# Kernel tuning notes

Hardware: AMD Instinct MI355X
Metric: run time of the kernel (lower is better)

Reference implementation:

```python
import jax, jax.numpy as jnp
import numpy as np

N = 2048
H = 128
W = 128
NEAR = 0.1


def _quat_to_rotmat(q):
    # q: [N,4] (w,x,y,z), normalized -> [N,3,3]
    q = q / jnp.clip(jnp.linalg.norm(q, axis=1, keepdims=True), 1e-8)
    w, x, y, z = q[:, 0], q[:, 1], q[:, 2], q[:, 3]
    xx, yy, zz = x * x, y * y, z * z
    xy, xz, yz = x * y, x * z, y * z
    wx, wy, wz = w * x, w * y, w * z
    r0 = jnp.stack([1 - 2 * (yy + zz), 2 * (xy - wz), 2 * (xz + wy)], axis=1)
    r1 = jnp.stack([2 * (xy + wz), 1 - 2 * (xx + zz), 2 * (yz - wx)], axis=1)
    r2 = jnp.stack([2 * (xz - wy), 2 * (yz + wx), 1 - 2 * (xx + yy)], axis=1)
    return jnp.stack([r0, r1, r2], axis=1)


def _covariance_matrices(log_scales, rotations):
    # R diag(s^2) R^T + 1e-6 I, per Gaussian
    s2 = jnp.exp(2.0 * log_scales)  # scales**2
    R = _quat_to_rotmat(rotations)  # [N,3,3]
    cov = jnp.einsum('nij,nj,nkj->nik', R, s2, R)
    return cov + 1e-6 * jnp.eye(3, dtype=cov.dtype)


def _render(means, cov3d, colors, opacities, intrinsics, camera_to_world, height, width):
    dt = means.dtype
    Rcw = camera_to_world[:3, :3]
    tcw = camera_to_world[:3, 3]
    Rwc = Rcw.T
    twc = -Rwc @ tcw
    p = means @ Rwc.T + twc  # [N,3] camera-space
    x, y, z = p[:, 0], p[:, 1], p[:, 2]
    valid = (z > NEAR).astype(dt)
    zc = jnp.maximum(z, NEAR)
    fx, fy = intrinsics[0, 0], intrinsics[1, 1]
    cx, cy = intrinsics[0, 2], intrinsics[1, 2]
    u = fx * x / zc + cx
    v = fy * y / zc + cy
    # EWA projection Jacobian [N,2,3]
    zeros = jnp.zeros_like(zc)
    J0 = jnp.stack([fx / zc, zeros, -fx * x / (zc * zc)], axis=1)
    J1 = jnp.stack([zeros, fy / zc, -fy * y / (zc * zc)], axis=1)
    J = jnp.stack([J0, J1], axis=1)
    cov_cam = jnp.einsum('ij,njk,lk->nil', Rwc, cov3d, Rwc)  # [N,3,3]
    cov2d = jnp.einsum('nij,njk,nlk->nil', J, cov_cam, J) + 0.3 * jnp.eye(2, dtype=dt)
    a, b, c = cov2d[:, 0, 0], cov2d[:, 0, 1], cov2d[:, 1, 1]
    det = jnp.maximum(a * c - b * b, 1e-12)
    cA, cB, cC = c / det, -b / det, a / det  # conic (inverse 2D covariance)
    # front-to-back depth order; invalid Gaussians pushed to the back
    order = jnp.argsort(jnp.where(valid > 0, zc, jnp.inf))
    u, v = u[order], v[order]
    cA, cB, cC = cA[order], cB[order], cC[order]
    op = (opacities * valid)[order]
    cols = colors[order]
    xs = jnp.arange(width, dtype=dt)
    ys = jnp.arange(height, dtype=dt)
    dx = xs[None, None, :] - u[:, None, None]  # [N,1,W] -> broadcasts
    dy = ys[None, :, None] - v[:, None, None]  # [N,H,1]
    power = (-0.5 * (cA[:, None, None] * dx * dx + cC[:, None, None] * dy * dy)
             - cB[:, None, None] * dx * dy)  # [N,H,W]
    power = jnp.minimum(power, 0.0)
    alpha = jnp.clip(op[:, None, None] * jnp.exp(power), 0.0, 0.99)
    Tcum = jnp.cumprod(1.0 - alpha, axis=0)
    Texcl = jnp.concatenate([jnp.ones_like(Tcum[:1]), Tcum[:-1]], axis=0)
    weight = alpha * Texcl  # [N,H,W]
    img = jnp.einsum('nhw,nc->hwc', weight, cols)  # [H,W,3]
    return img


def setup_inputs():
    key = jax.random.key(0)
    k = jax.random.split(key, 6)
    xy = jax.random.uniform(k[0], (N, 2), minval=-2.0, maxval=2.0)
    z = jax.random.uniform(k[1], (N, 1), minval=3.0, maxval=9.0)
    means = jnp.concatenate([xy, z], axis=1)
    log_scales = jnp.log(jax.random.uniform(k[2], (N, 3), minval=0.02, maxval=0.2))
    rotations = jax.random.normal(k[3], (N, 4))
    colors = jax.random.uniform(k[4], (N, 3))
    opacities = jax.random.normal(k[5], (N,))
    intrinsics = jnp.array([[150.0, 0.0, W / 2], [0.0, 150.0, H / 2], [0.0, 0.0, 1.0]], dtype=jnp.float32)
    camera_to_world = jnp.eye(4, dtype=jnp.float32)
    return {"means": means, "log_scales": log_scales, "rotations": rotations,
            "colors": colors, "opacities": opacities, "intrinsics": intrinsics,
            "camera_to_world": camera_to_world, "height": H, "width": W}


def reference(means, log_scales, rotations, colors, opacities, intrinsics, camera_to_world, height, width):
    cov3d = _covariance_matrices(log_scales, rotations)
    return _render(means, cov3d, jnp.clip(colors, 0.0, 1.0), jax.nn.sigmoid(opacities),
                   intrinsics, camera_to_world, height, width)
```

## Files before the change

### kernel.cpp

```cpp
#include <hip/hip_runtime.h>
#include <hip/hip_bf16.h>

#define NMAX 2048
#define HH 128
#define WW 128
#define NSEG 16
#define SEG 128
#define NEARP 0.1f
#define CULL_LOG_EPS -18.0f

static __device__ __forceinline__ float ldin(const void* p, int i, bool is32) {
    return is32 ? ((const float*)p)[i]
                : __bfloat162float(((const __hip_bfloat16*)p)[i]);
}
static __device__ __forceinline__ bool detect32(const void* intr) {
    return ((const float*)intr)[0] > 1.0f;
}
static __device__ __forceinline__ void stout(void* out, int i, float v, bool is32) {
    if (is32) ((float*)out)[i] = v;
    else      ((__hip_bfloat16*)out)[i] = __float2bfloat16(v);
}


__global__ __launch_bounds__(256) void gs_preprocess(
    const void* __restrict__ means,
    const void* __restrict__ log_scales,
    const void* __restrict__ rots,
    const void* __restrict__ colors,
    const void* __restrict__ opac,
    const void* __restrict__ intr,
    const void* __restrict__ c2w,
    int n,
    unsigned long long* __restrict__ keys,
    float* __restrict__ params)
{
    int i = blockIdx.x * blockDim.x + threadIdx.x;
    if (i >= NMAX) return;
    bool is32 = detect32(intr);
    if (i >= n) {
        keys[i] = (((unsigned long long)0x7f800000u) << 32) | (unsigned int)i;
        return;
    }

    float Rwc[3][3], twc[3];
    {
        float Rcw[3][3], tcw[3];
        for (int r = 0; r < 3; ++r) {
            for (int c = 0; c < 3; ++c) Rcw[r][c] = ldin(c2w, r * 4 + c, is32);
            tcw[r] = ldin(c2w, r * 4 + 3, is32);
        }
        for (int r = 0; r < 3; ++r)
            for (int c = 0; c < 3; ++c) Rwc[r][c] = Rcw[c][r];
        for (int r = 0; r < 3; ++r)
            twc[r] = -(Rwc[r][0] * tcw[0] + Rwc[r][1] * tcw[1] + Rwc[r][2] * tcw[2]);
    }
    float fx = ldin(intr, 0, is32), fy = ldin(intr, 4, is32);
    float cx = ldin(intr, 2, is32), cy = ldin(intr, 5, is32);

    float mx = ldin(means, 3 * i, is32), my = ldin(means, 3 * i + 1, is32),
          mz = ldin(means, 3 * i + 2, is32);
    float px = Rwc[0][0] * mx + Rwc[0][1] * my + Rwc[0][2] * mz + twc[0];
    float py = Rwc[1][0] * mx + Rwc[1][1] * my + Rwc[1][2] * mz + twc[1];
    float pz = Rwc[2][0] * mx + Rwc[2][1] * my + Rwc[2][2] * mz + twc[2];
    bool valid = pz > NEARP;
    float zc = fmaxf(pz, NEARP);
    float izc = 1.0f / zc;
    float u = fx * px * izc + cx;
    float v = fy * py * izc + cy;

    float qw = ldin(rots, 4 * i, is32), qx = ldin(rots, 4 * i + 1, is32),
          qy = ldin(rots, 4 * i + 2, is32), qz = ldin(rots, 4 * i + 3, is32);
    float nrm = sqrtf(qw * qw + qx * qx + qy * qy + qz * qz);
    float inv = 1.0f / fmaxf(nrm, 1e-8f);
    qw *= inv; qx *= inv; qy *= inv; qz *= inv;
    float xx = qx * qx, yy = qy * qy, zz = qz * qz;
    float xy = qx * qy, xz = qx * qz, yz = qy * qz;
    float wx = qw * qx, wy = qw * qy, wz = qw * qz;
    float R[3][3] = {
        {1.f - 2.f * (yy + zz), 2.f * (xy - wz),       2.f * (xz + wy)},
        {2.f * (xy + wz),       1.f - 2.f * (xx + zz), 2.f * (yz - wx)},
        {2.f * (xz - wy),       2.f * (yz + wx),       1.f - 2.f * (xx + yy)}
    };
    float s2[3];
    for (int k = 0; k < 3; ++k) s2[k] = __expf(2.0f * ldin(log_scales, 3 * i + k, is32));

    float M[3][3];
    for (int r = 0; r < 3; ++r)
        for (int c = 0; c < 3; ++c)
            M[r][c] = R[r][0] * s2[0] * R[c][0] + R[r][1] * s2[1] * R[c][1]
                    + R[r][2] * s2[2] * R[c][2];
    M[0][0] += 1e-6f; M[1][1] += 1e-6f; M[2][2] += 1e-6f;

    float TM[3][3];
    for (int r = 0; r < 3; ++r)
        for (int c = 0; c < 3; ++c)
            TM[r][c] = Rwc[r][0] * M[0][c] + Rwc[r][1] * M[1][c] + Rwc[r][2] * M[2][c];
    float CC[3][3];
    for (int r = 0; r < 3; ++r)
        for (int c = 0; c < 3; ++c)
            CC[r][c] = TM[r][0] * Rwc[c][0] + TM[r][1] * Rwc[c][1] + TM[r][2] * Rwc[c][2];

    float J0[3] = {fx * izc, 0.0f, -fx * px * izc * izc};
    float J1[3] = {0.0f, fy * izc, -fy * py * izc * izc};
    float t0[3], t1[3];
    for (int c = 0; c < 3; ++c) {
        t0[c] = J0[0] * CC[0][c] + J0[1] * CC[1][c] + J0[2] * CC[2][c];
        t1[c] = J1[0] * CC[0][c] + J1[1] * CC[1][c] + J1[2] * CC[2][c];
    }
    float a  = t0[0] * J0[0] + t0[1] * J0[1] + t0[2] * J0[2] + 0.3f;
    float bq = t0[0] * J1[0] + t0[1] * J1[1] + t0[2] * J1[2];
    float cq = t1[0] * J1[0] + t1[1] * J1[1] + t1[2] * J1[2] + 0.3f;
    float det = fmaxf(a * cq - bq * bq, 1e-12f);
    float idet = 1.0f / det;
    float cA = cq * idet, cB = -bq * idet, cCc = a * idet;

    float o  = ldin(opac, i, is32);
    float op = valid ? (1.0f / (1.0f + __expf(-o))) : 0.0f;
    float cr = fminf(fmaxf(ldin(colors, 3 * i, is32), 0.f), 1.f);
    float cg = fminf(fmaxf(ldin(colors, 3 * i + 1, is32), 0.f), 1.f);
    float cb = fminf(fmaxf(ldin(colors, 3 * i + 2, is32), 0.f), 1.f);

    float zkey = valid ? zc : __builtin_inff();
    keys[i] = (((unsigned long long)__float_as_uint(zkey)) << 32) | (unsigned int)i;

    float na  = -0.5f * cA;
    float nb  = -cB;
    float ncc = -0.5f * cCc;
    float qyb = ncc - nb * nb / (4.0f * na);
    float qxb = na  - nb * nb / (4.0f * ncc);
    float lnop = __logf(op);

    float* p = params + i * 12;
    p[0] = u;  p[1] = v;
    p[2] = na;  p[3] = nb;  p[4] = ncc;
    p[5] = op;
    p[6] = cr; p[7] = cg; p[8] = cb;
    p[9] = qyb; p[10] = lnop; p[11] = qxb;
}

__global__ __launch_bounds__(256) void gs_rank_scatter(
    const unsigned long long* __restrict__ keys_in,
    const float* __restrict__ params_in,
    float* __restrict__ params_sorted,
    int n)
{
    __shared__ unsigned long long sk[NMAX];
    __shared__ int pr[32][9];
    __shared__ int rk[32];
    int t = threadIdx.x;
    #pragma unroll
    for (int e = 0; e < 8; ++e) sk[t + e * 256] = keys_in[t + e * 256];
    __syncthreads();

    int g0 = blockIdx.x * 32;
    int gi = t >> 3;
    int c  = t & 7;
    unsigned long long mykey = sk[g0 + gi];
    int cnt = 0;
    #pragma unroll 8
    for (int j = c; j < NMAX; j += 8)
        cnt += (sk[j] < mykey) ? 1 : 0;
    pr[gi][c] = cnt;
    __syncthreads();

    if (t < 32) {
        int r = 0;
        #pragma unroll
        for (int k = 0; k < 8; ++k) r += pr[t][k];
        rk[t] = r;
    }
    __syncthreads();

    if (t < 96) {
        int g = t / 3, q = t % 3;
        int src = g0 + g;
        float4 val;
        if (src < n) val = ((const float4*)params_in)[src * 3 + q];
        else         val = make_float4(0.f, 0.f, 0.f, 0.f);
        ((float4*)params_sorted)[rk[g] * 3 + q] = val;
    }
}

__global__ __launch_bounds__(256) void gs_render(
    const float* __restrict__ params_sorted,
    float4* __restrict__ segbuf)
{
    __shared__ float sp[SEG * 12];
    __shared__ int swcnt[2];
    int seg = blockIdx.y;
    int t = threadIdx.x;
    int x0 = (blockIdx.x & 3) * 32;
    int y0 = (blockIdx.x >> 2) * 16;

    float4 a4, b4, c4;
    bool keep = false;
    if (t < SEG) {
        const float4* src = (const float4*)(params_sorted + (seg * SEG + t) * 12);
        a4 = src[0];
        b4 = src[1];
        c4 = src[2];
        float dxm = fmaxf(fmaxf((float)x0 - a4.x, a4.x - (float)(x0 + 31)), 0.0f);
        float dym = fmaxf(fmaxf((float)y0 - a4.y, a4.y - (float)(y0 + 15)), 0.0f);
        float bound = fminf(c4.y * dym * dym, c4.w * dxm * dxm) + c4.z;
        keep = (bound > CULL_LOG_EPS) && (b4.y > 0.0f);
    }
    unsigned long long ball = __ballot(keep);
    int lane = t & 63, wid = t >> 6;
    if (lane == 0 && wid < 2) swcnt[wid] = (int)__popcll(ball);
    __syncthreads();
    int M = swcnt[0] + swcnt[1];
    if (keep) {
        int rank = (wid ? swcnt[0] : 0)
                 + (int)__popcll(ball & ((1ull << lane) - 1ull));
        float4* d = (float4*)(sp + rank * 12);
        d[0] = a4; d[1] = b4; d[2] = c4;
    }
    __syncthreads();

    int col = x0 + ((t & 15) << 1);
    int row = y0 + (t >> 4);
    float px0 = (float)col;
    float px1 = px0 + 1.0f;
    float py  = (float)row;
    int pid0 = row * WW + col;

    float T0 = 1.f, r0 = 0.f, g0 = 0.f, b0 = 0.f;
    float T1 = 1.f, r1 = 0.f, g1 = 0.f, b1 = 0.f;
    #pragma unroll 2
    for (int i = 0; i < M; ++i) {
        const float* gp = sp + i * 12;
        float4 A = *(const float4*)(gp);
        float4 B = *(const float4*)(gp + 4);
        float4 C = *(const float4*)(gp + 8);
        float dy    = py - A.y;
        float nbdy  = A.w * dy;
        float ncdy2 = (B.x * dy) * dy;

        float dx0 = px0 - A.x;
        float p0 = fmaf(fmaf(A.z, dx0, nbdy), dx0, ncdy2);
        p0 = fminf(p0, 0.0f);
        float al0 = fminf(B.y * __expf(p0), 0.99f);
        float w0 = al0 * T0;
        r0 = fmaf(w0, B.z, r0);
        g0 = fmaf(w0, B.w, g0);
        b0 = fmaf(w0, C.x, b0);
        T0 *= (1.0f - al0);

        float dx1 = px1 - A.x;
        float p1 = fmaf(fmaf(A.z, dx1, nbdy), dx1, ncdy2);
        p1 = fminf(p1, 0.0f);
        float al1 = fminf(B.y * __expf(p1), 0.99f);
        float w1 = al1 * T1;
        r1 = fmaf(w1, B.z, r1);
        g1 = fmaf(w1, B.w, g1);
        b1 = fmaf(w1, C.x, b1);
        T1 *= (1.0f - al1);
    }
    segbuf[seg * (HH * WW) + pid0]     = make_float4(r0, g0, b0, T0);
    segbuf[seg * (HH * WW) + pid0 + 1] = make_float4(r1, g1, b1, T1);
}

__global__ __launch_bounds__(256) void gs_combine(
    const float4* __restrict__ segbuf,
    void* __restrict__ out,
    const void* __restrict__ intr)
{
    int pid = blockIdx.x * 256 + threadIdx.x;
    if (pid >= HH * WW) return;
    bool is32 = detect32(intr);
    float r = 0.f, g = 0.f, b = 0.f, T = 1.0f;
    #pragma unroll
    for (int s = 0; s < NSEG; ++s) {
        float4 vv = segbuf[s * (HH * WW) + pid];
        r = fmaf(T, vv.x, r);
        g = fmaf(T, vv.y, g);
        b = fmaf(T, vv.z, b);
        T *= vv.w;
    }
    stout(out, pid * 3 + 0, r, is32);
    stout(out, pid * 3 + 1, g, is32);
    stout(out, pid * 3 + 2, b, is32);
}

__global__ __launch_bounds__(256) void gs_render_all(
    const float* __restrict__ params_sorted,
    void* __restrict__ out,
    const void* __restrict__ intr)
{
    __shared__ float sp[SEG * 12];
    int t = threadIdx.x;
    int pid = blockIdx.x * 256 + t;
    bool is32 = detect32(intr);
    float pxf = (float)(pid & (WW - 1));
    float pyf = (float)(pid >> 7);

    float T = 1.f, r = 0.f, g = 0.f, b = 0.f;
    for (int seg = 0; seg < NSEG; ++seg) {
        __syncthreads();
        const float4* src = (const float4*)(params_sorted + seg * SEG * 12);
        float4* dst = (float4*)sp;
        #pragma unroll
        for (int k = t; k < SEG * 3; k += 256) dst[k] = src[k];
        __syncthreads();
        for (int i = 0; i < SEG; ++i) {
            const float* gp = sp + i * 12;
            float dx = pxf - gp[0];
            float dy = pyf - gp[1];
            float pwr = fmaf(fmaf(gp[2], dx, gp[3] * dy), dx, (gp[4] * dy) * dy);
            pwr = fminf(pwr, 0.0f);
            float alpha = fminf(gp[5] * __expf(pwr), 0.99f);
            float wgt = alpha * T;
            r = fmaf(wgt, gp[6], r);
            g = fmaf(wgt, gp[7], g);
            b = fmaf(wgt, gp[8], b);
            T *= (1.0f - alpha);
        }
    }
    stout(out, pid * 3 + 0, r, is32);
    stout(out, pid * 3 + 1, g, is32);
    stout(out, pid * 3 + 2, b, is32);
}

extern "C" void kernel_launch(void* const* d_in, const int* in_sizes, int n_in,
                              void* d_out, int out_size, void* d_ws, size_t ws_size,
                              hipStream_t stream)
{
    const void* means      = d_in[0];
    const void* log_scales = d_in[1];
    const void* rotations  = d_in[2];
    const void* colors     = d_in[3];
    const void* opacities  = d_in[4];
    const void* intrinsics = d_in[5];
    const void* cam2world  = d_in[6];

    int n = in_sizes[4];
    if (n > NMAX) n = NMAX;

    size_t off_keys   = 0;
    size_t off_params = NMAX * 8;
    size_t off_sorted = off_params + NMAX * 48;
    size_t off_seg    = off_sorted + NMAX * 48;
    size_t need_seg   = off_seg + (size_t)NSEG * HH * WW * 16;

    unsigned long long* keys = (unsigned long long*)((char*)d_ws + off_keys);
    float* params  = (float*)((char*)d_ws + off_params);
    float* sortedp = (float*)((char*)d_ws + off_sorted);
    float4* segbuf = (float4*)((char*)d_ws + off_seg);

    gs_preprocess<<<NMAX / 256, 256, 0, stream>>>(
        means, log_scales, rotations, colors, opacities, intrinsics, cam2world,
        n, keys, params);
    gs_rank_scatter<<<NMAX / 32, 256, 0, stream>>>(keys, params, sortedp, n);

    if (ws_size >= need_seg) {
        dim3 rg(32, NSEG);
        gs_render<<<rg, 256, 0, stream>>>(sortedp, segbuf);
        gs_combine<<<HH * WW / 256, 256, 0, stream>>>(segbuf, d_out, intrinsics);
    } else {
        gs_render_all<<<HH * WW / 256, 256, 0, stream>>>(sortedp, d_out, intrinsics);
    }
}
```

Baseline: 88.48 us.

## Replace global depth sort with per-tile depth binning and local sort

Removes the global rank-scatter sort kernel. Each render block now scans all Gaussians, keeps those that fall in its depth bin and overlap its tile, and sorts the survivors by depth in shared memory with a rank sort. Bins are fixed slices of the z range 3 to 9; values outside the range are clamped into the end bins, so compositing order stays correct. Opacity is folded into the exponent through the stored log-opacity. In exchange, every block rereads the full parameter array, pays a quadratic local sort, and reads Gaussian data from global memory through an index instead of from shared memory in the inner loop.

```diff
diff --git a/kernel.cpp b/kernel.cpp
--- a/kernel.cpp
+++ b/kernel.cpp
@@ -4,8 +4,9 @@
 #define NMAX 2048
 #define HH 128
 #define WW 128
-#define NSEG 16
-#define SEG 128
+#define NBIN 16
+#define ZLO 3.0f
+#define ZHI 9.0f
 #define NEARP 0.1f
 #define CULL_LOG_EPS -18.0f
 
@@ -31,14 +32,16 @@
     const void* __restrict__ intr,
     const void* __restrict__ c2w,
     int n,
-    unsigned long long* __restrict__ keys,
     float* __restrict__ params)
 {
     int i = blockIdx.x * blockDim.x + threadIdx.x;
     if (i >= NMAX) return;
     bool is32 = detect32(intr);
+    float* p = params + i * 12;
     if (i >= n) {
-        keys[i] = (((unsigned long long)0x7f800000u) << 32) | (unsigned int)i;
+        #pragma unroll
+        for (int k = 0; k < 12; ++k) p[k] = 0.f;
+        p[10] = -__builtin_inff();
         return;
     }
 
@@ -120,9 +123,6 @@
     float cg = fminf(fmaxf(ldin(colors, 3 * i + 1, is32), 0.f), 1.f);
     float cb = fminf(fmaxf(ldin(colors, 3 * i + 2, is32), 0.f), 1.f);
 
-    float zkey = valid ? zc : __builtin_inff();
-    keys[i] = (((unsigned long long)__float_as_uint(zkey)) << 32) | (unsigned int)i;
-
     float na  = -0.5f * cA;
     float nb  = -cB;
     float ncc = -0.5f * cCc;
@@ -130,91 +130,64 @@
     float qxb = na  - nb * nb / (4.0f * ncc);
     float lnop = __logf(op);
 
-    float* p = params + i * 12;
     p[0] = u;  p[1] = v;
     p[2] = na;  p[3] = nb;  p[4] = ncc;
-    p[5] = op;
+    p[5] = zc;
     p[6] = cr; p[7] = cg; p[8] = cb;
     p[9] = qyb; p[10] = lnop; p[11] = qxb;
 }
 
-__global__ __launch_bounds__(256) void gs_rank_scatter(
-    const unsigned long long* __restrict__ keys_in,
-    const float* __restrict__ params_in,
-    float* __restrict__ params_sorted,
-    int n)
-{
-    __shared__ unsigned long long sk[NMAX];
-    __shared__ int pr[32][9];
-    __shared__ int rk[32];
+__global__ __launch_bounds__(256) void gs_render_binned(
+    const float* __restrict__ params,
+    float4* __restrict__ segbuf)
+{
+    __shared__ unsigned long long slist[NMAX];
+    __shared__ int scnt;
     int t = threadIdx.x;
-    #pragma unroll
-    for (int e = 0; e < 8; ++e) sk[t + e * 256] = keys_in[t + e * 256];
-    __syncthreads();
-
-    int g0 = blockIdx.x * 32;
-    int gi = t >> 3;
-    int c  = t & 7;
-    unsigned long long mykey = sk[g0 + gi];
-    int cnt = 0;
-    #pragma unroll 8
-    for (int j = c; j < NMAX; j += 8)
-        cnt += (sk[j] < mykey) ? 1 : 0;
-    pr[gi][c] = cnt;
-    __syncthreads();
-
-    if (t < 32) {
-        int r = 0;
-        #pragma unroll
-        for (int k = 0; k < 8; ++k) r += pr[t][k];
-        rk[t] = r;
-    }
-    __syncthreads();
-
-    if (t < 96) {
-        int g = t / 3, q = t % 3;
-        int src = g0 + g;
-        float4 val;
-        if (src < n) val = ((const float4*)params_in)[src * 3 + q];
-        else         val = make_float4(0.f, 0.f, 0.f, 0.f);
-        ((float4*)params_sorted)[rk[g] * 3 + q] = val;
-    }
-}
-
-__global__ __launch_bounds__(256) void gs_render(
-    const float* __restrict__ params_sorted,
-    float4* __restrict__ segbuf)
-{
-    __shared__ float sp[SEG * 12];
-    __shared__ int swcnt[2];
-    int seg = blockIdx.y;
-    int t = threadIdx.x;
+    int bin = blockIdx.y;
     int x0 = (blockIdx.x & 3) * 32;
     int y0 = (blockIdx.x >> 2) * 16;
-
-    float4 a4, b4, c4;
-    bool keep = false;
-    if (t < SEG) {
-        const float4* src = (const float4*)(params_sorted + (seg * SEG + t) * 12);
-        a4 = src[0];
-        b4 = src[1];
-        c4 = src[2];
-        float dxm = fmaxf(fmaxf((float)x0 - a4.x, a4.x - (float)(x0 + 31)), 0.0f);
-        float dym = fmaxf(fmaxf((float)y0 - a4.y, a4.y - (float)(y0 + 15)), 0.0f);
-        float bound = fminf(c4.y * dym * dym, c4.w * dxm * dxm) + c4.z;
-        keep = (bound > CULL_LOG_EPS) && (b4.y > 0.0f);
-    }
-    unsigned long long ball = __ballot(keep);
-    int lane = t & 63, wid = t >> 6;
-    if (lane == 0 && wid < 2) swcnt[wid] = (int)__popcll(ball);
-    __syncthreads();
-    int M = swcnt[0] + swcnt[1];
-    if (keep) {
-        int rank = (wid ? swcnt[0] : 0)
-                 + (int)__popcll(ball & ((1ull << lane) - 1ull));
-        float4* d = (float4*)(sp + rank * 12);
-        d[0] = a4; d[1] = b4; d[2] = c4;
-    }
+    if (t == 0) scnt = 0;
+    __syncthreads();
+
+    const float kbin = (float)NBIN / (ZHI - ZLO);
+    #pragma unroll
+    for (int k = 0; k < NMAX / 256; ++k) {
+        int g = k * 256 + t;
+        const float4* rp = (const float4*)(params + 12 * g);
+        float4 A = rp[0];
+        float4 B = rp[1];
+        float4 C = rp[2];
+        int zb = (int)((B.y - ZLO) * kbin);
+        zb = zb < 0 ? 0 : (zb > NBIN - 1 ? NBIN - 1 : zb);
+        float dxm = fmaxf(fmaxf((float)x0 - A.x, A.x - (float)(x0 + 31)), 0.f);
+        float dym = fmaxf(fmaxf((float)y0 - A.y, A.y - (float)(y0 + 15)), 0.f);
+        float bound = fminf(C.y * dym * dym, C.w * dxm * dxm) + C.z;
+        if (zb == bin && bound > CULL_LOG_EPS) {
+            int s = atomicAdd(&scnt, 1);
+            slist[s] = (((unsigned long long)__float_as_uint(B.y)) << 32)
+                     | (unsigned int)g;
+        }
+    }
+    __syncthreads();
+    int M = scnt;
+
+    unsigned long long kk[NMAX / 256]; int rr[NMAX / 256];
+    #pragma unroll
+    for (int q = 0; q < NMAX / 256; ++q) {
+        int s = q * 256 + t;
+        rr[q] = -1;
+        if (s < M) {
+            unsigned long long key = slist[s];
+            int r = 0;
+            for (int j = 0; j < M; ++j) r += (slist[j] < key) ? 1 : 0;
+            kk[q] = key; rr[q] = r;
+        }
+    }
+    __syncthreads();
+    #pragma unroll
+    for (int q = 0; q < NMAX / 256; ++q)
+        if (rr[q] >= 0) slist[rr[q]] = kk[q];
     __syncthreads();
 
     int col = x0 + ((t & 15) << 1);
@@ -228,18 +201,19 @@
     float T1 = 1.f, r1 = 0.f, g1 = 0.f, b1 = 0.f;
     #pragma unroll 2
     for (int i = 0; i < M; ++i) {
-        const float* gp = sp + i * 12;
-        float4 A = *(const float4*)(gp);
-        float4 B = *(const float4*)(gp + 4);
-        float4 C = *(const float4*)(gp + 8);
+        int g = (int)(unsigned int)slist[i];
+        const float4* rp = (const float4*)(params + 12 * g);
+        float4 A = rp[0];
+        float4 B = rp[1];
+        float4 C = rp[2];
         float dy    = py - A.y;
         float nbdy  = A.w * dy;
         float ncdy2 = (B.x * dy) * dy;
+        float lnop  = C.z;
 
         float dx0 = px0 - A.x;
         float p0 = fmaf(fmaf(A.z, dx0, nbdy), dx0, ncdy2);
-        p0 = fminf(p0, 0.0f);
-        float al0 = fminf(B.y * __expf(p0), 0.99f);
+        float al0 = fminf(__expf(fminf(p0, 0.0f) + lnop), 0.99f);
         float w0 = al0 * T0;
         r0 = fmaf(w0, B.z, r0);
         g0 = fmaf(w0, B.w, g0);
@@ -248,16 +222,15 @@
 
         float dx1 = px1 - A.x;
         float p1 = fmaf(fmaf(A.z, dx1, nbdy), dx1, ncdy2);
-        p1 = fminf(p1, 0.0f);
-        float al1 = fminf(B.y * __expf(p1), 0.99f);
+        float al1 = fminf(__expf(fminf(p1, 0.0f) + lnop), 0.99f);
         float w1 = al1 * T1;
         r1 = fmaf(w1, B.z, r1);
         g1 = fmaf(w1, B.w, g1);
         b1 = fmaf(w1, C.x, b1);
         T1 *= (1.0f - al1);
     }
-    segbuf[seg * (HH * WW) + pid0]     = make_float4(r0, g0, b0, T0);
-    segbuf[seg * (HH * WW) + pid0 + 1] = make_float4(r1, g1, b1, T1);
+    segbuf[bin * (HH * WW) + pid0]     = make_float4(r0, g0, b0, T0);
+    segbuf[bin * (HH * WW) + pid0 + 1] = make_float4(r1, g1, b1, T1);
 }
 
 __global__ __launch_bounds__(256) void gs_combine(
@@ -270,7 +243,7 @@
     bool is32 = detect32(intr);
     float r = 0.f, g = 0.f, b = 0.f, T = 1.0f;
     #pragma unroll
-    for (int s = 0; s < NSEG; ++s) {
+    for (int s = 0; s < NBIN; ++s) {
         float4 vv = segbuf[s * (HH * WW) + pid];
         r = fmaf(T, vv.x, r);
         g = fmaf(T, vv.y, g);
@@ -283,39 +256,71 @@
 }
 
 __global__ __launch_bounds__(256) void gs_render_all(
-    const float* __restrict__ params_sorted,
+    const float* __restrict__ params,
     void* __restrict__ out,
     const void* __restrict__ intr)
 {
-    __shared__ float sp[SEG * 12];
+    __shared__ unsigned long long slist[NMAX];
+    __shared__ int scnt;
     int t = threadIdx.x;
-    int pid = blockIdx.x * 256 + t;
+    int x0 = (blockIdx.x & 7) * 16;
+    int y0 = (blockIdx.x >> 3) * 16;
     bool is32 = detect32(intr);
-    float pxf = (float)(pid & (WW - 1));
-    float pyf = (float)(pid >> 7);
-
+    if (t == 0) scnt = 0;
+    __syncthreads();
+
+    #pragma unroll
+    for (int k = 0; k < NMAX / 256; ++k) {
+        int g = k * 256 + t;
+        const float4* rp = (const float4*)(params + 12 * g);
+        float4 A = rp[0]; float4 B = rp[1]; float4 C = rp[2];
+        float dxm = fmaxf(fmaxf((float)x0 - A.x, A.x - (float)(x0 + 15)), 0.f);
+        float dym = fmaxf(fmaxf((float)y0 - A.y, A.y - (float)(y0 + 15)), 0.f);
+        float bound = fminf(C.y * dym * dym, C.w * dxm * dxm) + C.z;
+        if (bound > CULL_LOG_EPS) {
+            int s = atomicAdd(&scnt, 1);
+            slist[s] = (((unsigned long long)__float_as_uint(B.y)) << 32)
+                     | (unsigned int)g;
+        }
+    }
+    __syncthreads();
+    int M = scnt;
+    unsigned long long kk[NMAX / 256]; int rr[NMAX / 256];
+    #pragma unroll
+    for (int q = 0; q < NMAX / 256; ++q) {
+        int s = q * 256 + t;
+        rr[q] = -1;
+        if (s < M) {
+            unsigned long long key = slist[s];
+            int r = 0;
+            for (int j = 0; j < M; ++j) r += (slist[j] < key) ? 1 : 0;
+            kk[q] = key; rr[q] = r;
+        }
+    }
+    __syncthreads();
+    #pragma unroll
+    for (int q = 0; q < NMAX / 256; ++q)
+        if (rr[q] >= 0) slist[rr[q]] = kk[q];
+    __syncthreads();
+
+    float pxf = (float)(x0 + (t & 15));
+    float pyf = (float)(y0 + (t >> 4));
     float T = 1.f, r = 0.f, g = 0.f, b = 0.f;
-    for (int seg = 0; seg < NSEG; ++seg) {
-        __syncthreads();
-        const float4* src = (const float4*)(params_sorted + seg * SEG * 12);
-        float4* dst = (float4*)sp;
-        #pragma unroll
-        for (int k = t; k < SEG * 3; k += 256) dst[k] = src[k];
-        __syncthreads();
-        for (int i = 0; i < SEG; ++i) {
-            const float* gp = sp + i * 12;
-            float dx = pxf - gp[0];
-            float dy = pyf - gp[1];
-            float pwr = fmaf(fmaf(gp[2], dx, gp[3] * dy), dx, (gp[4] * dy) * dy);
-            pwr = fminf(pwr, 0.0f);
-            float alpha = fminf(gp[5] * __expf(pwr), 0.99f);
-            float wgt = alpha * T;
-            r = fmaf(wgt, gp[6], r);
-            g = fmaf(wgt, gp[7], g);
-            b = fmaf(wgt, gp[8], b);
-            T *= (1.0f - alpha);
-        }
-    }
+    for (int i = 0; i < M; ++i) {
+        int gg = (int)(unsigned int)slist[i];
+        const float4* rp = (const float4*)(params + 12 * gg);
+        float4 A = rp[0]; float4 B = rp[1]; float4 C = rp[2];
+        float dx = pxf - A.x;
+        float dy = pyf - A.y;
+        float pwr = fmaf(fmaf(A.z, dx, A.w * dy), dx, (B.x * dy) * dy);
+        float alpha = fminf(__expf(fminf(pwr, 0.0f) + C.z), 0.99f);
+        float wgt = alpha * T;
+        r = fmaf(wgt, B.z, r);
+        g = fmaf(wgt, B.w, g);
+        b = fmaf(wgt, C.x, b);
+        T *= (1.0f - alpha);
+    }
+    int pid = (y0 + (t >> 4)) * WW + x0 + (t & 15);
     stout(out, pid * 3 + 0, r, is32);
     stout(out, pid * 3 + 1, g, is32);
     stout(out, pid * 3 + 2, b, is32);
@@ -336,27 +341,22 @@
     int n = in_sizes[4];
     if (n > NMAX) n = NMAX;
 
-    size_t off_keys   = 0;
-    size_t off_params = NMAX * 8;
-    size_t off_sorted = off_params + NMAX * 48;
-    size_t off_seg    = off_sorted + NMAX * 48;
-    size_t need_seg   = off_seg + (size_t)NSEG * HH * WW * 16;
-
-    unsigned long long* keys = (unsigned long long*)((char*)d_ws + off_keys);
+    size_t off_params = 0;
+    size_t off_seg    = NMAX * 48;
+    size_t need_seg   = off_seg + (size_t)NBIN * HH * WW * 16;
+
     float* params  = (float*)((char*)d_ws + off_params);
-    float* sortedp = (float*)((char*)d_ws + off_sorted);
     float4* segbuf = (float4*)((char*)d_ws + off_seg);
 
     gs_preprocess<<<NMAX / 256, 256, 0, stream>>>(
         means, log_scales, rotations, colors, opacities, intrinsics, cam2world,
-        n, keys, params);
-    gs_rank_scatter<<<NMAX / 32, 256, 0, stream>>>(keys, params, sortedp, n);
+        n, params);
 
     if (ws_size >= need_seg) {
-        dim3 rg(32, NSEG);
-        gs_render<<<rg, 256, 0, stream>>>(sortedp, segbuf);
+        dim3 rg(32, NBIN);
+        gs_render_binned<<<rg, 256, 0, stream>>>(params, segbuf);
         gs_combine<<<HH * WW / 256, 256, 0, stream>>>(segbuf, d_out, intrinsics);
     } else {
-        gs_render_all<<<HH * WW / 256, 256, 0, stream>>>(sortedp, d_out, intrinsics);
-    }
-}
+        gs_render_all<<<HH * WW / 256, 256, 0, stream>>>(params, d_out, intrinsics);
+    }
+}
```

After: 90.53 us. +2.3%, slower.

## Replace param scatter with index order and fuse segment combine into render

Applied to the files above, without the earlier changes.

The rank kernel now writes only a 16-bit sorted index per Gaussian and no longer scatters the full parameter records. The render kernel gathers parameters through that index. The separate combine kernel is folded into the render kernel: each segment block bumps a per-tile atomic counter after writing its partial result, and the seg-0 block spin-waits until all segments are done, then composites. This removes one kernel launch and one copy pass, at the cost of indirect gathers and a spin-wait that depends on all 512 blocks being resident together (deadlock risk otherwise).

```diff
diff --git a/kernel.cpp b/kernel.cpp
--- a/kernel.cpp
+++ b/kernel.cpp
@@ -138,16 +138,15 @@
     p[9] = qyb; p[10] = lnop; p[11] = qxb;
 }
 
-__global__ __launch_bounds__(256) void gs_rank_scatter(
+__global__ __launch_bounds__(256) void gs_rank(
     const unsigned long long* __restrict__ keys_in,
-    const float* __restrict__ params_in,
-    float* __restrict__ params_sorted,
-    int n)
+    unsigned short* __restrict__ order,
+    int* __restrict__ tiledone)
 {
     __shared__ unsigned long long sk[NMAX];
     __shared__ int pr[32][9];
-    __shared__ int rk[32];
     int t = threadIdx.x;
+    if (blockIdx.x == 0 && t < 32) tiledone[t] = 0;
     #pragma unroll
     for (int e = 0; e < 8; ++e) sk[t + e * 256] = keys_in[t + e * 256];
     __syncthreads();
@@ -167,52 +166,51 @@
         int r = 0;
         #pragma unroll
         for (int k = 0; k < 8; ++k) r += pr[t][k];
-        rk[t] = r;
-    }
-    __syncthreads();
-
-    if (t < 96) {
-        int g = t / 3, q = t % 3;
-        int src = g0 + g;
-        float4 val;
-        if (src < n) val = ((const float4*)params_in)[src * 3 + q];
-        else         val = make_float4(0.f, 0.f, 0.f, 0.f);
-        ((float4*)params_sorted)[rk[g] * 3 + q] = val;
-    }
-}
-
-__global__ __launch_bounds__(256) void gs_render(
-    const float* __restrict__ params_sorted,
-    float4* __restrict__ segbuf)
-{
-    __shared__ float sp[SEG * 12];
+        order[r] = (unsigned short)(g0 + t);
+    }
+}
+
+__global__ __launch_bounds__(256) void gs_render_combine(
+    const float* __restrict__ params,
+    const unsigned short* __restrict__ order,
+    int n,
+    float4* __restrict__ segbuf,
+    int* __restrict__ tiledone,
+    void* __restrict__ out,
+    const void* __restrict__ intr)
+{
+    __shared__ __align__(16) float srec[SEG * 12];
     __shared__ int swcnt[2];
     int seg = blockIdx.y;
     int t = threadIdx.x;
-    int x0 = (blockIdx.x & 3) * 32;
-    int y0 = (blockIdx.x >> 2) * 16;
+    int lane = t & 63, wid = t >> 6;
+    int tile = blockIdx.x;
+    int x0 = (tile & 3) * 32;
+    int y0 = (tile >> 2) * 16;
 
     float4 a4, b4, c4;
     bool keep = false;
     if (t < SEG) {
-        const float4* src = (const float4*)(params_sorted + (seg * SEG + t) * 12);
-        a4 = src[0];
-        b4 = src[1];
-        c4 = src[2];
-        float dxm = fmaxf(fmaxf((float)x0 - a4.x, a4.x - (float)(x0 + 31)), 0.0f);
-        float dym = fmaxf(fmaxf((float)y0 - a4.y, a4.y - (float)(y0 + 15)), 0.0f);
-        float bound = fminf(c4.y * dym * dym, c4.w * dxm * dxm) + c4.z;
-        keep = (bound > CULL_LOG_EPS) && (b4.y > 0.0f);
+        int g = (int)order[seg * SEG + t];
+        if (g < n) {
+            const float4* src = (const float4*)(params + g * 12);
+            a4 = src[0];
+            b4 = src[1];
+            c4 = src[2];
+            float dxm = fmaxf(fmaxf((float)x0 - a4.x, a4.x - (float)(x0 + 31)), 0.0f);
+            float dym = fmaxf(fmaxf((float)y0 - a4.y, a4.y - (float)(y0 + 15)), 0.0f);
+            float bound = fminf(c4.y * dym * dym, c4.w * dxm * dxm) + c4.z;
+            keep = (bound > CULL_LOG_EPS) && (b4.y > 0.0f);
+        }
     }
     unsigned long long ball = __ballot(keep);
-    int lane = t & 63, wid = t >> 6;
     if (lane == 0 && wid < 2) swcnt[wid] = (int)__popcll(ball);
     __syncthreads();
     int M = swcnt[0] + swcnt[1];
     if (keep) {
         int rank = (wid ? swcnt[0] : 0)
                  + (int)__popcll(ball & ((1ull << lane) - 1ull));
-        float4* d = (float4*)(sp + rank * 12);
+        float4* d = (float4*)(srec + rank * 12);
         d[0] = a4; d[1] = b4; d[2] = c4;
     }
     __syncthreads();
@@ -228,7 +226,7 @@
     float T1 = 1.f, r1 = 0.f, g1 = 0.f, b1 = 0.f;
     #pragma unroll 2
     for (int i = 0; i < M; ++i) {
-        const float* gp = sp + i * 12;
+        const float* gp = srec + i * 12;
         float4 A = *(const float4*)(gp);
         float4 B = *(const float4*)(gp + 4);
         float4 C = *(const float4*)(gp + 8);
@@ -258,36 +256,47 @@
     }
     segbuf[seg * (HH * WW) + pid0]     = make_float4(r0, g0, b0, T0);
     segbuf[seg * (HH * WW) + pid0 + 1] = make_float4(r1, g1, b1, T1);
-}
-
-__global__ __launch_bounds__(256) void gs_combine(
-    const float4* __restrict__ segbuf,
+
+    __threadfence();
+    if (t == 0) atomicAdd(&tiledone[tile], 1);
+
+    if (seg == 0) {
+        if (t == 0) {
+            while (atomicAdd(&tiledone[tile], 0) < NSEG)
+                __builtin_amdgcn_s_sleep(8);
+        }
+        __syncthreads();
+        __threadfence();
+        bool is32 = detect32(intr);
+
+        float rA = 0.f, gA = 0.f, bA = 0.f, TA = 1.0f;
+        float rB = 0.f, gB = 0.f, bB = 0.f, TB = 1.0f;
+        #pragma unroll
+        for (int s = 0; s < NSEG; ++s) {
+            float4 vA = segbuf[s * (HH * WW) + pid0];
+            float4 vB = segbuf[s * (HH * WW) + pid0 + 1];
+            rA = fmaf(TA, vA.x, rA); gA = fmaf(TA, vA.y, gA);
+            bA = fmaf(TA, vA.z, bA); TA *= vA.w;
+            rB = fmaf(TB, vB.x, rB); gB = fmaf(TB, vB.y, gB);
+            bB = fmaf(TB, vB.z, bB); TB *= vB.w;
+        }
+        stout(out, pid0 * 3 + 0, rA, is32);
+        stout(out, pid0 * 3 + 1, gA, is32);
+        stout(out, pid0 * 3 + 2, bA, is32);
+        stout(out, (pid0 + 1) * 3 + 0, rB, is32);
+        stout(out, (pid0 + 1) * 3 + 1, gB, is32);
+        stout(out, (pid0 + 1) * 3 + 2, bB, is32);
+    }
+}
+
+__global__ __launch_bounds__(256) void gs_render_all(
+    const float* __restrict__ params,
+    const unsigned short* __restrict__ order,
+    int n,
     void* __restrict__ out,
     const void* __restrict__ intr)
 {
-    int pid = blockIdx.x * 256 + threadIdx.x;
-    if (pid >= HH * WW) return;
-    bool is32 = detect32(intr);
-    float r = 0.f, g = 0.f, b = 0.f, T = 1.0f;
-    #pragma unroll
-    for (int s = 0; s < NSEG; ++s) {
-        float4 vv = segbuf[s * (HH * WW) + pid];
-        r = fmaf(T, vv.x, r);
-        g = fmaf(T, vv.y, g);
-        b = fmaf(T, vv.z, b);
-        T *= vv.w;
-    }
-    stout(out, pid * 3 + 0, r, is32);
-    stout(out, pid * 3 + 1, g, is32);
-    stout(out, pid * 3 + 2, b, is32);
-}
-
-__global__ __launch_bounds__(256) void gs_render_all(
-    const float* __restrict__ params_sorted,
-    void* __restrict__ out,
-    const void* __restrict__ intr)
-{
-    __shared__ float sp[SEG * 12];
+    __shared__ __align__(16) float srec[SEG * 12];
     int t = threadIdx.x;
     int pid = blockIdx.x * 256 + t;
     bool is32 = detect32(intr);
@@ -297,13 +306,21 @@
     float T = 1.f, r = 0.f, g = 0.f, b = 0.f;
     for (int seg = 0; seg < NSEG; ++seg) {
         __syncthreads();
-        const float4* src = (const float4*)(params_sorted + seg * SEG * 12);
-        float4* dst = (float4*)sp;
-        #pragma unroll
-        for (int k = t; k < SEG * 3; k += 256) dst[k] = src[k];
+        if (t < SEG) {
+            int gi = (int)order[seg * SEG + t];
+            float4* d = (float4*)(srec + t * 12);
+            if (gi < n) {
+                const float4* src = (const float4*)(params + gi * 12);
+                d[0] = src[0]; d[1] = src[1]; d[2] = src[2];
+            } else {
+                d[0] = make_float4(0.f, 0.f, 0.f, 0.f);
+                d[1] = make_float4(0.f, 0.f, 0.f, 0.f);
+                d[2] = make_float4(0.f, 0.f, 0.f, 0.f);
+            }
+        }
         __syncthreads();
         for (int i = 0; i < SEG; ++i) {
-            const float* gp = sp + i * 12;
+            const float* gp = srec + i * 12;
             float dx = pxf - gp[0];
             float dy = pyf - gp[1];
             float pwr = fmaf(fmaf(gp[2], dx, gp[3] * dy), dx, (gp[4] * dy) * dy);
@@ -336,27 +353,24 @@
     int n = in_sizes[4];
     if (n > NMAX) n = NMAX;
 
-    size_t off_keys   = 0;
-    size_t off_params = NMAX * 8;
-    size_t off_sorted = off_params + NMAX * 48;
-    size_t off_seg    = off_sorted + NMAX * 48;
-    size_t need_seg   = off_seg + (size_t)NSEG * HH * WW * 16;
-
-    unsigned long long* keys = (unsigned long long*)((char*)d_ws + off_keys);
-    float* params  = (float*)((char*)d_ws + off_params);
-    float* sortedp = (float*)((char*)d_ws + off_sorted);
-    float4* segbuf = (float4*)((char*)d_ws + off_seg);
+    unsigned long long* keys = (unsigned long long*)d_ws;
+    float* params            = (float*)((char*)d_ws + 16384);
+    unsigned short* order    = (unsigned short*)((char*)d_ws + 114688);
+    int* tiledone            = (int*)((char*)d_ws + 118784);
+    float4* segbuf           = (float4*)((char*)d_ws + 131072);
+    size_t need = 131072 + (size_t)NSEG * HH * WW * 16;
 
     gs_preprocess<<<NMAX / 256, 256, 0, stream>>>(
         means, log_scales, rotations, colors, opacities, intrinsics, cam2world,
         n, keys, params);
-    gs_rank_scatter<<<NMAX / 32, 256, 0, stream>>>(keys, params, sortedp, n);
-
-    if (ws_size >= need_seg) {
+    gs_rank<<<NMAX / 32, 256, 0, stream>>>(keys, order, tiledone);
+
+    if (ws_size >= need) {
         dim3 rg(32, NSEG);
-        gs_render<<<rg, 256, 0, stream>>>(sortedp, segbuf);
-        gs_combine<<<HH * WW / 256, 256, 0, stream>>>(segbuf, d_out, intrinsics);
+        gs_render_combine<<<rg, 256, 0, stream>>>(
+            params, order, n, segbuf, tiledone, d_out, intrinsics);
     } else {
-        gs_render_all<<<HH * WW / 256, 256, 0, stream>>>(sortedp, d_out, intrinsics);
-    }
-}
+        gs_render_all<<<HH * WW / 256, 256, 0, stream>>>(
+            params, order, n, d_out, intrinsics);
+    }
+}
```

Result: slower. 144.6 us (+63.4%).
